# Kernel tuning notes

Hardware: AMD Instinct MI355X
Metric: run time of the kernel (lower is better)

Reference implementation:

```python
import jax, jax.numpy as jnp
import numpy as np

TOKEN_DIM = 256
NUM_HEADS = 2
IN_DIMS = 512
D = TOKEN_DIM * NUM_HEADS  # 512
SCALE = TOKEN_DIM ** (-0.5)


def _l2norm(v, axis):
    # torch F.normalize: v / max(||v||_2, eps)
    n = jnp.sqrt(jnp.sum(v * v, axis=axis, keepdims=True))
    return v / jnp.maximum(n, 1e-12)


def setup_inputs() -> dict:
    key = jax.random.key(0)
    ks = jax.random.split(key, 10)
    b, n = 8, 4096
    x = jax.random.normal(ks[0], (b, n, IN_DIMS), dtype=jnp.float32)
    s = 0.02
    Wq = jax.random.normal(ks[1], (IN_DIMS, D), dtype=jnp.float32) * s
    bq = jax.random.normal(ks[2], (D,), dtype=jnp.float32) * s
    Wk = jax.random.normal(ks[3], (IN_DIMS, D), dtype=jnp.float32) * s
    bk = jax.random.normal(ks[4], (D,), dtype=jnp.float32) * s
    Wr = jax.random.normal(ks[5], (D, TOKEN_DIM), dtype=jnp.float32) * s
    br = jax.random.normal(ks[6], (TOKEN_DIM,), dtype=jnp.float32) * s
    w_alpha = jax.random.normal(ks[7], (D, 1), dtype=jnp.float32)
    w_beta = jax.random.normal(ks[8], (D, 1), dtype=jnp.float32)
    return {"x": x, "Wq": Wq, "bq": bq, "Wk": Wk, "bk": bk,
            "Wr": Wr, "br": br, "w_alpha": w_alpha, "w_beta": w_beta}


def reference(x, Wq, bq, Wk, bk, Wr, br, w_alpha, w_beta):
    # x: [b, n, in_dims]
    q = x @ Wq + bq                      # [b, n, D]
    k = x @ Wk + bk                      # [b, n, D]
    q = _l2norm(q, axis=-1)
    k = _l2norm(k, axis=-1)
    v = _l2norm(k, axis=-1)              # original bug: value = normalize(key)

    alpha_w = (q @ w_alpha) * SCALE      # [b, n, 1]
    alpha_w = _l2norm(alpha_w, axis=1)   # normalize over token axis
    g_q = jnp.sum(alpha_w * q, axis=1)   # [b, D]
    g_q = jax.nn.softmax(g_q, axis=-1)

    p = g_q[:, None, :] * k              # [b, n, D]
    beta_w = _l2norm((p @ w_beta) * SCALE, axis=1)  # [b, n, 1]
    g_k = jnp.sum(beta_w * p, axis=1)    # [b, D]
    g_k = jax.nn.softmax(g_k, axis=-1)

    kvi = g_k[:, None, :] * v + q        # [b, n, D]
    return kvi @ Wr + br                 # [b, n, token_dim]
```

## Files before the change

kernel.cpp:

```cpp
#include <hip/hip_runtime.h>
#include <hip/hip_bf16.h>
#include <stdint.h>

#define BATCH    8
#define NTOKB    4096
#define NTOK     (BATCH * NTOKB)
#define DIN      512
#define DD       512
#define TD       256
#define SCALE    0.0625f
#define LSTR     36
#define LSTR2    68

typedef unsigned short ushortT;
typedef __attribute__((ext_vector_type(8))) short  short8;
typedef __attribute__((ext_vector_type(4))) float  f32x4;

union Frag { uint4 u; short8 s; };

__device__ __forceinline__ float bf_lo(uint32_t u) { return __uint_as_float(u << 16); }
__device__ __forceinline__ float bf_hi(uint32_t u) { return __uint_as_float(u & 0xffff0000u); }
__device__ __forceinline__ ushortT f2bf(float f) {
    uint32_t u = __float_as_uint(f);
    return (ushortT)((u + 0x7fffu + ((u >> 16) & 1u)) >> 16);
}
__device__ __forceinline__ short8 lds_frag(const ushortT* p) {
    uint2 a = *reinterpret_cast<const uint2*>(p);
    uint2 b = *reinterpret_cast<const uint2*>(p + 4);
    Frag f; f.u.x = a.x; f.u.y = a.y; f.u.z = b.x; f.u.w = b.y;
    return f.s;
}
__device__ __forceinline__ void gload_lds16(const ushortT* g, ushortT* l) {
    __builtin_amdgcn_global_load_lds(
        (const __attribute__((address_space(1))) uint32_t*)(const void*)g,
        (__attribute__((address_space(3))) uint32_t*)(void*)l,
        16, 0, 0);
}

__global__ __launch_bounds__(256) void packw_kernel(
    const float* __restrict__ Wq, const float* __restrict__ Wk,
    const float* __restrict__ Wr, ushortT* __restrict__ W16)
{
    const int blk = blockIdx.x;
    if (blk < 32) {
        const int mat = blk >> 4, c = blk & 15;
        const float* S = mat ? Wk : Wq;
        ushortT* D = W16 + (size_t)mat * (512 * 512) + (size_t)(c >> 1) * 32768;
        const int khalf = c & 1;
        for (int i = threadIdx.x; i < 16384; i += 256) {
            int n = i & 511, q = i >> 9;
            int l = khalf * 4 + (q >> 3);
            int p = l ^ ((n >> 1) & 7);
            D[n * 64 + p * 8 + (q & 7)] = f2bf(S[(size_t)(c * 32 + q) * 512 + n]);
        }
    } else {
        const int c = blk - 32;
        ushortT* D = W16 + (size_t)2 * (512 * 512) + (size_t)c * 8192;
        for (int i = threadIdx.x; i < 8192; i += 256) {
            int n = i & 255, p = i >> 8;
            int l = ((p >> 3) ^ ((n >> 1) & 3)) * 8 + (p & 7);
            D[n * 32 + p] = f2bf(Wr[(size_t)(c * 32 + l) * 256 + n]);
        }
    }
}

__global__ __launch_bounds__(512) void gemm_qk_kernel(
    const float* __restrict__ x, const ushortT* __restrict__ W16,
    const float* __restrict__ bq, const float* __restrict__ bk,
    const float* __restrict__ w_alpha,
    ushortT* __restrict__ qn, ushortT* __restrict__ kn,
    float* __restrict__ alpha_raw, float* __restrict__ gq_raw)
{
    __shared__ __align__(16) ushortT xs[64 * LSTR2];
    __shared__ __align__(16) ushortT wsd[512 * 64];
    __shared__ float rowsq[8][64];
    __shared__ float alphap[8][64];
    __shared__ float rnorm_s[64];
    __shared__ float alpha_sh[64];

    const int tid = threadIdx.x;
    const int mat = blockIdx.y;
    const size_t tok0 = (size_t)blockIdx.x * 64;
    const int b = (int)(blockIdx.x >> 6);
    const ushortT* Wb = W16 + (size_t)mat * (512 * 512);
    const float* bias = mat ? bk : bq;
    ushortT* dst = mat ? kn : qn;

    const int lane = tid & 63, w = tid >> 6;
    const int m = lane & 15, quad = lane >> 4;

    f32x4 acc[4][4];
    #pragma unroll
    for (int tr = 0; tr < 4; ++tr)
        #pragma unroll
        for (int tc = 0; tc < 4; ++tc) acc[tr][tc] = (f32x4){0.f, 0.f, 0.f, 0.f};

    const int xtok = tid >> 3;
    const int xkg  = (tid & 7) * 8;
    const float* xsrc = x + (tok0 + xtok) * DIN;

    for (int c = 0; c < 8; ++c) {
        __syncthreads();
        {
            float4 v0 = *reinterpret_cast<const float4*>(xsrc + c * 64 + xkg);
            float4 v1 = *reinterpret_cast<const float4*>(xsrc + c * 64 + xkg + 4);
            ushort4 b0, b1;
            b0.x = f2bf(v0.x); b0.y = f2bf(v0.y); b0.z = f2bf(v0.z); b0.w = f2bf(v0.w);
            b1.x = f2bf(v1.x); b1.y = f2bf(v1.y); b1.z = f2bf(v1.z); b1.w = f2bf(v1.w);
            *reinterpret_cast<ushort4*>(&xs[xtok * LSTR2 + xkg]) = b0;
            *reinterpret_cast<ushort4*>(&xs[xtok * LSTR2 + xkg + 4]) = b1;
        }
        {
            const ushortT* wsrc = Wb + (size_t)c * 32768;
            #pragma unroll
            for (int i = 0; i < 8; ++i) {
                const int region = i * 8 + w;
                gload_lds16(wsrc + region * 512 + lane * 8, &wsd[region * 512]);
            }
        }
        __syncthreads();
        #pragma unroll
        for (int kk = 0; kk < 2; ++kk) {
            short8 af[4], bfv[4];
            #pragma unroll
            for (int tr = 0; tr < 4; ++tr)
                af[tr] = lds_frag(&xs[(tr * 16 + m) * LSTR2 + kk * 32 + quad * 8]);
            #pragma unroll
            for (int tc = 0; tc < 4; ++tc) {
                const int n = w * 64 + tc * 16 + m;
                const int p = (kk * 4 + quad) ^ ((n >> 1) & 7);
                bfv[tc] = *reinterpret_cast<const short8*>(&wsd[n * 64 + p * 8]);
            }
            #pragma unroll
            for (int tr = 0; tr < 4; ++tr)
                #pragma unroll
                for (int tc = 0; tc < 4; ++tc)
                    acc[tr][tc] = __builtin_amdgcn_mfma_f32_16x16x32_bf16(af[tr], bfv[tc], acc[tr][tc], 0, 0, 0);
        }
    }

    float biasv[4], wa[4];
    #pragma unroll
    for (int tc = 0; tc < 4; ++tc) {
        biasv[tc] = bias[w * 64 + tc * 16 + m];
        wa[tc] = (mat == 0) ? w_alpha[w * 64 + tc * 16 + m] : 0.f;
    }
    #pragma unroll
    for (int tr = 0; tr < 4; ++tr)
        #pragma unroll
        for (int tc = 0; tc < 4; ++tc)
            #pragma unroll
            for (int reg = 0; reg < 4; ++reg)
                acc[tr][tc][reg] += biasv[tc];

    __syncthreads();
    #pragma unroll
    for (int tr = 0; tr < 4; ++tr) {
        #pragma unroll
        for (int reg = 0; reg < 4; ++reg) {
            float s = 0.f, a = 0.f;
            #pragma unroll
            for (int tc = 0; tc < 4; ++tc) {
                float v = acc[tr][tc][reg];
                s = fmaf(v, v, s);
                a = fmaf(v, wa[tc], a);
            }
            #pragma unroll
            for (int off = 1; off < 16; off <<= 1) {
                s += __shfl_xor(s, off);
                a += __shfl_xor(a, off);
            }
            if (m == 0) {
                rowsq[w][tr * 16 + quad * 4 + reg] = s;
                alphap[w][tr * 16 + quad * 4 + reg] = a;
            }
        }
    }
    __syncthreads();
    if (tid < 64) {
        float ss = 0.f, aa = 0.f;
        #pragma unroll
        for (int w2 = 0; w2 < 8; ++w2) { ss += rowsq[w2][tid]; aa += alphap[w2][tid]; }
        float rn = 1.0f / fmaxf(sqrtf(ss), 1e-12f);
        float av = SCALE * aa * rn;
        rnorm_s[tid] = rn;
        alpha_sh[tid] = av;
        if (mat == 0) alpha_raw[tok0 + tid] = av;
    }
    __syncthreads();
    float gqp[4] = {0.f, 0.f, 0.f, 0.f};
    #pragma unroll
    for (int tr = 0; tr < 4; ++tr) {
        #pragma unroll
        for (int reg = 0; reg < 4; ++reg) {
            const int rloc = tr * 16 + quad * 4 + reg;
            float rn = rnorm_s[rloc];
            float av = alpha_sh[rloc];
            size_t row = tok0 + rloc;
            ushortT* rp = dst + row * DD + w * 64 + m;
            #pragma unroll
            for (int tc = 0; tc < 4; ++tc) {
                float val = acc[tr][tc][reg] * rn;
                rp[tc * 16] = f2bf(val);
                gqp[tc] = fmaf(av, val, gqp[tc]);
            }
        }
    }
    if (mat == 0) {
        #pragma unroll
        for (int tc = 0; tc < 4; ++tc) {
            float p = gqp[tc];
            p += __shfl_xor(p, 16);
            p += __shfl_xor(p, 32);
            if (quad == 0)
                atomicAdd(&gq_raw[b * DD + w * 64 + tc * 16 + m], p);
        }
    }
}

__global__ __launch_bounds__(256) void fused_softmax_kernel(
    const float* __restrict__ nrm_in, const float* __restrict__ in,
    const float* __restrict__ mul, const float* __restrict__ wbeta,
    float* __restrict__ out, float* __restrict__ wb2)
{
    int b = blockIdx.x, tid = threadIdx.x;
    __shared__ float red[256];
    float s = 0.f;
    for (int i = tid; i < NTOKB; i += 256) {
        float v = nrm_in[b * NTOKB + i];
        s = fmaf(v, v, s);
    }
    red[tid] = s;
    __syncthreads();
    for (int off = 128; off > 0; off >>= 1) {
        if (tid < off) red[tid] += red[tid + off];
        __syncthreads();
    }
    float inv = 1.0f / fmaxf(sqrtf(red[0]), 1e-12f);
    __syncthreads();
    float v0 = in[b * DD + tid] * inv, v1 = in[b * DD + 256 + tid] * inv;
    if (mul) { v0 *= mul[b * DD + tid]; v1 *= mul[b * DD + 256 + tid]; }
    red[tid] = fmaxf(v0, v1);
    __syncthreads();
    for (int off = 128; off > 0; off >>= 1) {
        if (tid < off) red[tid] = fmaxf(red[tid], red[tid + off]);
        __syncthreads();
    }
    float m = red[0];
    __syncthreads();
    float e0 = expf(v0 - m), e1 = expf(v1 - m);
    red[tid] = e0 + e1;
    __syncthreads();
    for (int off = 128; off > 0; off >>= 1) {
        if (tid < off) red[tid] += red[tid + off];
        __syncthreads();
    }
    float rs = 1.0f / red[0];
    float o0 = e0 * rs, o1 = e1 * rs;
    out[b * DD + tid] = o0;
    out[b * DD + 256 + tid] = o1;
    if (wb2) {
        wb2[b * DD + tid]       = o0 * wbeta[tid];
        wb2[b * DD + 256 + tid] = o1 * wbeta[256 + tid];
    }
}

__global__ __launch_bounds__(256) void betawsum_kernel(
    const ushortT* __restrict__ kn, const float* __restrict__ wb2,
    float* __restrict__ beta_raw, float* __restrict__ h_raw)
{
    const int blk = blockIdx.x, tid = threadIdx.x;
    const int b = blk >> 6;
    const int i0 = (blk & 63) * 64;
    __shared__ float bs[64];

    const int wave = tid >> 6, lane = tid & 63;
    float4 wv0 = *reinterpret_cast<const float4*>(wb2 + b * DD + lane * 8);
    float4 wv1 = *reinterpret_cast<const float4*>(wb2 + b * DD + lane * 8 + 4);

    for (int it = 0; it < 16; ++it) {
        const int t = it * 4 + wave;
        const size_t tok = (size_t)b * NTOKB + i0 + t;
        uint4 kv = *reinterpret_cast<const uint4*>(kn + tok * DD + lane * 8);
        float s = bf_lo(kv.x) * wv0.x + bf_hi(kv.x) * wv0.y
                + bf_lo(kv.y) * wv0.z + bf_hi(kv.y) * wv0.w
                + bf_lo(kv.z) * wv1.x + bf_hi(kv.z) * wv1.y
                + bf_lo(kv.w) * wv1.z + bf_hi(kv.w) * wv1.w;
        #pragma unroll
        for (int off = 32; off > 0; off >>= 1) s += __shfl_xor(s, off);
        if (lane == 0) {
            float bv = SCALE * s;
            bs[t] = bv;
            beta_raw[tok] = bv;
        }
    }
    __syncthreads();

    const uint32_t* M32 = reinterpret_cast<const uint32_t*>(kn);
    size_t base = ((size_t)b * NTOKB + i0) * 256 + tid;
    float a0 = 0.f, a1 = 0.f;
    for (int ii = 0; ii < 64; ++ii) {
        uint32_t v = M32[base + (size_t)ii * 256];
        float wv = bs[ii];
        a0 = fmaf(wv, bf_lo(v), a0);
        a1 = fmaf(wv, bf_hi(v), a1);
    }
    atomicAdd(&h_raw[b * DD + 2 * tid],     a0);
    atomicAdd(&h_raw[b * DD + 2 * tid + 1], a1);
}

__global__ __launch_bounds__(256) void out_mfma_kernel(
    const ushortT* __restrict__ qn, const ushortT* __restrict__ kn,
    const float* __restrict__ g_k, const ushortT* __restrict__ WrT,
    const float* __restrict__ br, float* __restrict__ out)
{
    __shared__ __align__(16) ushortT kvs[64 * LSTR];
    __shared__ __align__(16) ushortT wrs[256 * 32];
    __shared__ float gks[512];

    const int tid = threadIdx.x;
    const size_t tok0 = (size_t)blockIdx.x * 64;
    const int b = (int)(tok0 >> 12);

    gks[tid] = g_k[b * DD + tid];
    gks[256 + tid] = g_k[b * DD + 256 + tid];

    const int lane = tid & 63, w = tid >> 6;
    const int m = lane & 15, quad = lane >> 4;

    f32x4 acc[4][4];
    #pragma unroll
    for (int tr = 0; tr < 4; ++tr)
        #pragma unroll
        for (int tc = 0; tc < 4; ++tc) acc[tr][tc] = (f32x4){0.f, 0.f, 0.f, 0.f};

    const int st  = tid >> 2;
    const int skg = (tid & 3) * 8;

    for (int c = 0; c < 16; ++c) {
        __syncthreads();
        {
            const size_t base = (tok0 + st) * DD + c * 32 + skg;
            uint4 qv = *reinterpret_cast<const uint4*>(qn + base);
            uint4 kv = *reinterpret_cast<const uint4*>(kn + base);
            const float* g = &gks[c * 32 + skg];
            ushortT o[8];
            o[0] = f2bf(fmaf(g[0], bf_lo(kv.x), bf_lo(qv.x)));
            o[1] = f2bf(fmaf(g[1], bf_hi(kv.x), bf_hi(qv.x)));
            o[2] = f2bf(fmaf(g[2], bf_lo(kv.y), bf_lo(qv.y)));
            o[3] = f2bf(fmaf(g[3], bf_hi(kv.y), bf_hi(qv.y)));
            o[4] = f2bf(fmaf(g[4], bf_lo(kv.z), bf_lo(qv.z)));
            o[5] = f2bf(fmaf(g[5], bf_hi(kv.z), bf_hi(qv.z)));
            o[6] = f2bf(fmaf(g[6], bf_lo(kv.w), bf_lo(qv.w)));
            o[7] = f2bf(fmaf(g[7], bf_hi(kv.w), bf_hi(qv.w)));
            uint2* lp = reinterpret_cast<uint2*>(&kvs[st * LSTR + skg]);
            lp[0] = make_uint2(((uint32_t)o[1] << 16) | o[0], ((uint32_t)o[3] << 16) | o[2]);
            lp[1] = make_uint2(((uint32_t)o[5] << 16) | o[4], ((uint32_t)o[7] << 16) | o[6]);
        }
        {
            const ushortT* wsrc = WrT + (size_t)c * 8192;
            #pragma unroll
            for (int i = 0; i < 4; ++i) {
                const int region = i * 4 + w;
                gload_lds16(wsrc + region * 512 + lane * 8, &wrs[region * 512]);
            }
        }
        __syncthreads();
        {
            short8 af[4], bfr[4];
            #pragma unroll
            for (int tr = 0; tr < 4; ++tr)
                af[tr] = lds_frag(&kvs[(tr * 16 + m) * LSTR + quad * 8]);
            #pragma unroll
            for (int tc = 0; tc < 4; ++tc) {
                const int n = w * 64 + tc * 16 + m;
                bfr[tc] = *reinterpret_cast<const short8*>(
                    &wrs[n * 32 + ((quad ^ ((n >> 1) & 3)) * 8)]);
            }
            #pragma unroll
            for (int tr = 0; tr < 4; ++tr)
                #pragma unroll
                for (int tc = 0; tc < 4; ++tc)
                    acc[tr][tc] = __builtin_amdgcn_mfma_f32_16x16x32_bf16(af[tr], bfr[tc], acc[tr][tc], 0, 0, 0);
        }
    }

    float brv[4];
    #pragma unroll
    for (int tc = 0; tc < 4; ++tc) brv[tc] = br[w * 64 + tc * 16 + m];
    #pragma unroll
    for (int tr = 0; tr < 4; ++tr) {
        #pragma unroll
        for (int reg = 0; reg < 4; ++reg) {
            size_t row = tok0 + tr * 16 + quad * 4 + reg;
            float* rp = out + row * TD + w * 64 + m;
            #pragma unroll
            for (int tc = 0; tc < 4; ++tc)
                rp[tc * 16] = acc[tr][tc][reg] + brv[tc];
        }
    }
}

extern "C" void kernel_launch(void* const* d_in, const int* in_sizes, int n_in,
                              void* d_out, int out_size, void* d_ws, size_t ws_size,
                              hipStream_t stream)
{
    const float* x       = (const float*)d_in[0];
    const float* Wq      = (const float*)d_in[1];
    const float* bq      = (const float*)d_in[2];
    const float* Wk      = (const float*)d_in[3];
    const float* bk      = (const float*)d_in[4];
    const float* Wr      = (const float*)d_in[5];
    const float* br      = (const float*)d_in[6];
    const float* w_alpha = (const float*)d_in[7];
    const float* w_beta  = (const float*)d_in[8];
    float* out = (float*)d_out;

    ushortT* kn = (ushortT*)d_out;

    char* ws = (char*)d_ws;
    ushortT* qn = (ushortT*)ws;        ws += (size_t)NTOK * DD * sizeof(ushortT);
    ushortT* W16 = (ushortT*)ws;       ws += (size_t)2 * 512 * 512 * sizeof(ushortT)
                                           + (size_t)512 * 256 * sizeof(ushortT);
    float* alpha_raw = (float*)ws;     ws += (size_t)NTOK * sizeof(float);
    float* beta_raw  = (float*)ws;     ws += (size_t)NTOK * sizeof(float);
    float* gq_raw = (float*)ws;        ws += (size_t)BATCH * DD * sizeof(float);
    float* h_raw  = (float*)ws;        ws += (size_t)BATCH * DD * sizeof(float);
    float* g_q    = (float*)ws;        ws += (size_t)BATCH * DD * sizeof(float);
    float* wb2    = (float*)ws;        ws += (size_t)BATCH * DD * sizeof(float);
    float* g_k    = (float*)ws;        ws += (size_t)BATCH * DD * sizeof(float);
    ushortT* WrT = W16 + (size_t)2 * 512 * 512;

    hipMemsetAsync(gq_raw, 0, 2 * BATCH * DD * sizeof(float), stream);

    packw_kernel<<<48, 256, 0, stream>>>(Wq, Wk, Wr, W16);
    gemm_qk_kernel<<<dim3(NTOK / 64, 2), 512, 0, stream>>>(x, W16, bq, bk, w_alpha,
                                                           qn, kn, alpha_raw, gq_raw);
    fused_softmax_kernel<<<BATCH, 256, 0, stream>>>(alpha_raw, gq_raw, nullptr,
                                                    w_beta, g_q, wb2);
    betawsum_kernel<<<NTOK / 64, 256, 0, stream>>>(kn, wb2, beta_raw, h_raw);
    fused_softmax_kernel<<<BATCH, 256, 0, stream>>>(beta_raw, h_raw, g_q,
                                                    nullptr, g_k, nullptr);
    out_mfma_kernel<<<NTOK / 64, 256, 0, stream>>>(qn, kn, g_k, WrT, br, out);
}
```

Baseline: 234.8 us.

## Fold softmax stages into consumer kernels by recomputing per block

Removes the two small 8-block softmax kernels and instead has every block of betawsum and out_mfma redo the token-axis norm reduction and softmax for its batch. This drops two kernel launches and the round trips through g_q, wb2 and g_k workspace buffers. In exchange, each of the 512 blocks rereads 4096 (or 8192) floats and runs many barrier-heavy reductions before its main work, which is redundant compute repeated in every block.

```diff
diff --git a/kernel.cpp b/kernel.cpp
--- a/kernel.cpp
+++ b/kernel.cpp
@@ -218,65 +218,57 @@
     }
 }
 
-__global__ __launch_bounds__(256) void fused_softmax_kernel(
-    const float* __restrict__ nrm_in, const float* __restrict__ in,
-    const float* __restrict__ mul, const float* __restrict__ wbeta,
-    float* __restrict__ out, float* __restrict__ wb2)
-{
-    int b = blockIdx.x, tid = threadIdx.x;
-    __shared__ float red[256];
-    float s = 0.f;
-    for (int i = tid; i < NTOKB; i += 256) {
-        float v = nrm_in[b * NTOKB + i];
-        s = fmaf(v, v, s);
-    }
-    red[tid] = s;
-    __syncthreads();
-    for (int off = 128; off > 0; off >>= 1) {
-        if (tid < off) red[tid] += red[tid + off];
-        __syncthreads();
-    }
-    float inv = 1.0f / fmaxf(sqrtf(red[0]), 1e-12f);
-    __syncthreads();
-    float v0 = in[b * DD + tid] * inv, v1 = in[b * DD + 256 + tid] * inv;
-    if (mul) { v0 *= mul[b * DD + tid]; v1 *= mul[b * DD + 256 + tid]; }
-    red[tid] = fmaxf(v0, v1);
-    __syncthreads();
-    for (int off = 128; off > 0; off >>= 1) {
-        if (tid < off) red[tid] = fmaxf(red[tid], red[tid + off]);
-        __syncthreads();
-    }
-    float m = red[0];
-    __syncthreads();
-    float e0 = expf(v0 - m), e1 = expf(v1 - m);
-    red[tid] = e0 + e1;
-    __syncthreads();
-    for (int off = 128; off > 0; off >>= 1) {
-        if (tid < off) red[tid] += red[tid + off];
-        __syncthreads();
-    }
-    float rs = 1.0f / red[0];
-    float o0 = e0 * rs, o1 = e1 * rs;
-    out[b * DD + tid] = o0;
-    out[b * DD + 256 + tid] = o1;
-    if (wb2) {
-        wb2[b * DD + tid]       = o0 * wbeta[tid];
-        wb2[b * DD + 256 + tid] = o1 * wbeta[256 + tid];
-    }
-}
-
 __global__ __launch_bounds__(256) void betawsum_kernel(
-    const ushortT* __restrict__ kn, const float* __restrict__ wb2,
+    const ushortT* __restrict__ kn, const float* __restrict__ alpha_raw,
+    const float* __restrict__ gq_raw, const float* __restrict__ w_beta,
     float* __restrict__ beta_raw, float* __restrict__ h_raw)
 {
     const int blk = blockIdx.x, tid = threadIdx.x;
     const int b = blk >> 6;
     const int i0 = (blk & 63) * 64;
+    __shared__ float red[256];
+    __shared__ float wb2s[512];
     __shared__ float bs[64];
 
+    {
+        float s = 0.f;
+        for (int i = tid; i < NTOKB; i += 256) {
+            float v = alpha_raw[b * NTOKB + i];
+            s = fmaf(v, v, s);
+        }
+        red[tid] = s;
+        __syncthreads();
+        for (int off = 128; off > 0; off >>= 1) {
+            if (tid < off) red[tid] += red[tid + off];
+            __syncthreads();
+        }
+        float inv = 1.0f / fmaxf(sqrtf(red[0]), 1e-12f);
+        __syncthreads();
+        float v0 = gq_raw[b * DD + tid] * inv, v1 = gq_raw[b * DD + 256 + tid] * inv;
+        red[tid] = fmaxf(v0, v1);
+        __syncthreads();
+        for (int off = 128; off > 0; off >>= 1) {
+            if (tid < off) red[tid] = fmaxf(red[tid], red[tid + off]);
+            __syncthreads();
+        }
+        float m = red[0];
+        __syncthreads();
+        float e0 = expf(v0 - m), e1 = expf(v1 - m);
+        red[tid] = e0 + e1;
+        __syncthreads();
+        for (int off = 128; off > 0; off >>= 1) {
+            if (tid < off) red[tid] += red[tid + off];
+            __syncthreads();
+        }
+        float rs = 1.0f / red[0];
+        wb2s[tid]       = (e0 * rs) * w_beta[tid];
+        wb2s[256 + tid] = (e1 * rs) * w_beta[256 + tid];
+    }
+    __syncthreads();
+
     const int wave = tid >> 6, lane = tid & 63;
-    float4 wv0 = *reinterpret_cast<const float4*>(wb2 + b * DD + lane * 8);
-    float4 wv1 = *reinterpret_cast<const float4*>(wb2 + b * DD + lane * 8 + 4);
+    float4 wv0 = *reinterpret_cast<const float4*>(&wb2s[lane * 8]);
+    float4 wv1 = *reinterpret_cast<const float4*>(&wb2s[lane * 8 + 4]);
 
     for (int it = 0; it < 16; ++it) {
         const int t = it * 4 + wave;
@@ -311,19 +303,85 @@
 
 __global__ __launch_bounds__(256) void out_mfma_kernel(
     const ushortT* __restrict__ qn, const ushortT* __restrict__ kn,
-    const float* __restrict__ g_k, const ushortT* __restrict__ WrT,
-    const float* __restrict__ br, float* __restrict__ out)
+    const float* __restrict__ alpha_raw, const float* __restrict__ beta_raw,
+    const float* __restrict__ gq_raw, const float* __restrict__ h_raw,
+    const ushortT* __restrict__ WrT, const float* __restrict__ br,
+    float* __restrict__ out)
 {
     __shared__ __align__(16) ushortT kvs[64 * LSTR];
     __shared__ __align__(16) ushortT wrs[256 * 32];
     __shared__ float gks[512];
+    __shared__ float red[256];
 
     const int tid = threadIdx.x;
     const size_t tok0 = (size_t)blockIdx.x * 64;
     const int b = (int)(tok0 >> 12);
 
-    gks[tid] = g_k[b * DD + tid];
-    gks[256 + tid] = g_k[b * DD + 256 + tid];
+    {
+        float sa = 0.f, sb = 0.f;
+        for (int i = tid; i < NTOKB; i += 256) {
+            float va = alpha_raw[b * NTOKB + i];
+            float vb = beta_raw[b * NTOKB + i];
+            sa = fmaf(va, va, sa);
+            sb = fmaf(vb, vb, sb);
+        }
+        red[tid] = sa;
+        __syncthreads();
+        for (int off = 128; off > 0; off >>= 1) {
+            if (tid < off) red[tid] += red[tid + off];
+            __syncthreads();
+        }
+        float inv_a = 1.0f / fmaxf(sqrtf(red[0]), 1e-12f);
+        __syncthreads();
+        red[tid] = sb;
+        __syncthreads();
+        for (int off = 128; off > 0; off >>= 1) {
+            if (tid < off) red[tid] += red[tid + off];
+            __syncthreads();
+        }
+        float inv_b = 1.0f / fmaxf(sqrtf(red[0]), 1e-12f);
+        __syncthreads();
+        float q0 = gq_raw[b * DD + tid] * inv_a, q1 = gq_raw[b * DD + 256 + tid] * inv_a;
+        red[tid] = fmaxf(q0, q1);
+        __syncthreads();
+        for (int off = 128; off > 0; off >>= 1) {
+            if (tid < off) red[tid] = fmaxf(red[tid], red[tid + off]);
+            __syncthreads();
+        }
+        float m1 = red[0];
+        __syncthreads();
+        float eq0 = expf(q0 - m1), eq1 = expf(q1 - m1);
+        red[tid] = eq0 + eq1;
+        __syncthreads();
+        for (int off = 128; off > 0; off >>= 1) {
+            if (tid < off) red[tid] += red[tid + off];
+            __syncthreads();
+        }
+        float rsq = 1.0f / red[0];
+        float gq0 = eq0 * rsq, gq1 = eq1 * rsq;
+        __syncthreads();
+        float h0 = h_raw[b * DD + tid] * inv_b;
+        float h1 = h_raw[b * DD + 256 + tid] * inv_b;
+        h0 *= gq0; h1 *= gq1;
+        red[tid] = fmaxf(h0, h1);
+        __syncthreads();
+        for (int off = 128; off > 0; off >>= 1) {
+            if (tid < off) red[tid] = fmaxf(red[tid], red[tid + off]);
+            __syncthreads();
+        }
+        float m2 = red[0];
+        __syncthreads();
+        float eh0 = expf(h0 - m2), eh1 = expf(h1 - m2);
+        red[tid] = eh0 + eh1;
+        __syncthreads();
+        for (int off = 128; off > 0; off >>= 1) {
+            if (tid < off) red[tid] += red[tid + off];
+            __syncthreads();
+        }
+        float rsk = 1.0f / red[0];
+        gks[tid]       = eh0 * rsk;
+        gks[256 + tid] = eh1 * rsk;
+    }
 
     const int lane = tid & 63, w = tid >> 6;
     const int m = lane & 15, quad = lane >> 4;
@@ -426,9 +484,6 @@
     float* beta_raw  = (float*)ws;     ws += (size_t)NTOK * sizeof(float);
     float* gq_raw = (float*)ws;        ws += (size_t)BATCH * DD * sizeof(float);
     float* h_raw  = (float*)ws;        ws += (size_t)BATCH * DD * sizeof(float);
-    float* g_q    = (float*)ws;        ws += (size_t)BATCH * DD * sizeof(float);
-    float* wb2    = (float*)ws;        ws += (size_t)BATCH * DD * sizeof(float);
-    float* g_k    = (float*)ws;        ws += (size_t)BATCH * DD * sizeof(float);
     ushortT* WrT = W16 + (size_t)2 * 512 * 512;
 
     hipMemsetAsync(gq_raw, 0, 2 * BATCH * DD * sizeof(float), stream);
@@ -436,10 +491,8 @@
     packw_kernel<<<48, 256, 0, stream>>>(Wq, Wk, Wr, W16);
     gemm_qk_kernel<<<dim3(NTOK / 64, 2), 512, 0, stream>>>(x, W16, bq, bk, w_alpha,
                                                            qn, kn, alpha_raw, gq_raw);
-    fused_softmax_kernel<<<BATCH, 256, 0, stream>>>(alpha_raw, gq_raw, nullptr,
-                                                    w_beta, g_q, wb2);
-    betawsum_kernel<<<NTOK / 64, 256, 0, stream>>>(kn, wb2, beta_raw, h_raw);
-    fused_softmax_kernel<<<BATCH, 256, 0, stream>>>(beta_raw, h_raw, g_q,
-                                                    nullptr, g_k, nullptr);
-    out_mfma_kernel<<<NTOK / 64, 256, 0, stream>>>(qn, kn, g_k, WrT, br, out);
-}
+    betawsum_kernel<<<NTOK / 64, 256, 0, stream>>>(kn, alpha_raw, gq_raw, w_beta,
+                                                   beta_raw, h_raw);
+    out_mfma_kernel<<<NTOK / 64, 256, 0, stream>>>(qn, kn, alpha_raw, beta_raw,
+                                                   gq_raw, h_raw, WrT, br, out);
+}
```

Result: no change. 233.4 us (-0.6%).
